# Performance work log

Hardware: AMD Instinct MI355X
Metric: run time of the kernel (lower is better)

The kernel has to match this reference:

```python
import jax, jax.numpy as jnp
import numpy as np

WCNT, EMB, H, T, B = 50000, 25, 25, 200, 4096


def setup_inputs() -> dict:
    key = jax.random.key(0)
    ks = jax.random.split(key, 12)
    s = 1.0 / np.sqrt(H)  # PyTorch GRU init range

    def u(k, shape):
        return jax.random.uniform(k, shape, minval=-s, maxval=s, dtype=jnp.float32)

    emb = jax.random.normal(ks[1], (WCNT, EMB), dtype=jnp.float32)
    emb = emb.at[0].set(0.0)  # padding_idx=0
    return {
        "input": jax.random.randint(ks[0], (T, B), 0, WCNT),
        "hidden": jnp.zeros((2, B, H), jnp.float32),
        "emb": emb,
        "w_ih_f": u(ks[2], (3 * H, EMB)), "w_hh_f": u(ks[3], (3 * H, H)),
        "b_ih_f": u(ks[4], (3 * H,)),     "b_hh_f": u(ks[5], (3 * H,)),
        "w_ih_b": u(ks[6], (3 * H, EMB)), "w_hh_b": u(ks[7], (3 * H, H)),
        "b_ih_b": u(ks[8], (3 * H,)),     "b_hh_b": u(ks[9], (3 * H,)),
    }


def _gru_dir(x, h0, w_ih, w_hh, b_ih, b_hh, reverse):
    # Precompute input-gate projections for all timesteps: [T, B, 3H]
    xg = jnp.einsum('tbi,gi->tbg', x, w_ih) + b_ih

    def step(h, xg_t):
        gh = h @ w_hh.T + b_hh
        xr, xz, xn = jnp.split(xg_t, 3, axis=-1)
        hr, hz, hn = jnp.split(gh, 3, axis=-1)
        r = jax.nn.sigmoid(xr + hr)
        z = jax.nn.sigmoid(xz + hz)
        n = jnp.tanh(xn + r * hn)
        h_new = (1.0 - z) * n + z * h
        return h_new, h_new

    hT, ys = jax.lax.scan(step, h0, xg, reverse=reverse)
    return ys, hT  # ys in original time order even when reversed


def reference(input, hidden, emb,
              w_ih_f, w_hh_f, b_ih_f, b_hh_f,
              w_ih_b, w_hh_b, b_ih_b, b_hh_b):
    emb_eff = emb.at[0].set(0.0)          # padding_idx=0
    x = emb_eff[input]                    # [T, B, EMB]
    yf, hf = _gru_dir(x, hidden[0], w_ih_f, w_hh_f, b_ih_f, b_hh_f, False)
    yb, hb = _gru_dir(x, hidden[1], w_ih_b, w_hh_b, b_ih_b, b_hh_b, True)
    y = jnp.concatenate([yf, yb], axis=-1)  # [T, B, 2H]
    y = jnp.max(y, axis=0)                  # max over time -> [B, 2H]
    h = jnp.stack([hf, hb], axis=0)         # [2, B, H]
    return (y, h)
```

## Files before the change

kernel.cpp:

```cpp
#include <hip/hip_runtime.h>
#include <cstddef>

#define T_LEN 200
#define BATCH 4096
#define EMBD  25
#define HD    25
#define WCNT  50000

__device__ __forceinline__ float frcp(float x) {
#if __has_builtin(__builtin_amdgcn_rcpf)
    return __builtin_amdgcn_rcpf(x);
#else
    return 1.0f / x;
#endif
}

__device__ __forceinline__ float fsig(float x) {
    float e = __expf(-x);
    return frcp(1.0f + e);
}
__device__ __forceinline__ float ftanh_(float x) {
    float e = __expf(-2.0f * x);
    return (1.0f - e) * frcp(1.0f + e);
}

__global__ __launch_bounds__(256) void embp_kernel(
    const float* __restrict__ emb,
    const float* __restrict__ w_ih_f, const float* __restrict__ b_ih_f,
    const float* __restrict__ w_ih_b, const float* __restrict__ b_ih_b,
    float* __restrict__ embP)
{
    int tid = blockIdx.x * 256 + threadIdx.x;
    if (tid >= 2 * WCNT * HD) return;
    int i   = tid % HD;
    int w   = (tid / HD) % WCNT;
    int dir = tid / (HD * WCNT);
    const float* wih = dir ? w_ih_b : w_ih_f;
    const float* bih = dir ? b_ih_b : b_ih_f;
    const float* er  = emb + (size_t)w * EMBD;
    const float* w0  = wih + (0 * HD + i) * EMBD;
    const float* w1  = wih + (1 * HD + i) * EMBD;
    const float* w2  = wih + (2 * HD + i) * EMBD;
    float a0 = bih[i], a1 = bih[HD + i], a2 = bih[2 * HD + i];
    #pragma unroll
    for (int j = 0; j < EMBD; ++j) {
        float x = er[j];
        a0 = fmaf(w0[j], x, a0);
        a1 = fmaf(w1[j], x, a1);
        a2 = fmaf(w2[j], x, a2);
    }
    float* o = embP + ((size_t)dir * WCNT + w) * 75;
    o[i] = a0; o[i + 25] = a1; o[i + 50] = a2;
}

template<bool USE_EMBP>
__global__ __launch_bounds__(256) void gru_kernel(
    const int*   __restrict__ input,
    const float* __restrict__ hidden,
    const float* __restrict__ emb,
    const float* __restrict__ w_hh_f, const float* __restrict__ b_hh_f,
    const float* __restrict__ w_ih_f, const float* __restrict__ b_ih_f,
    const float* __restrict__ w_hh_b, const float* __restrict__ b_hh_b,
    const float* __restrict__ w_ih_b, const float* __restrict__ b_ih_b,
    const float* __restrict__ embP,
    float* __restrict__ out)
{
    __shared__ float4 hsh4[8][7];
    __shared__ float4 xsh4[8][7];
    float* hshf = (float*)hsh4;
    float* xshf = (float*)xsh4;

    const int wave = threadIdx.x >> 6;
    const int half = (threadIdx.x >> 5) & 1;
    const int sub  = threadIdx.x & 31;
    const int b    = blockIdx.x * 4 + wave;
    const int dir  = half;
    const int csub = sub < 25 ? sub : 0;
    const int c    = wave * 2 + half;

    const float* whh = dir ? w_hh_b : w_hh_f;
    const float* bhh = dir ? b_hh_b : b_hh_f;
    const float* wih = dir ? w_ih_b : w_ih_f;
    const float* bih = dir ? b_ih_b : b_ih_f;

    float wg0[28], wg1[28], wg2[28];
    #pragma unroll
    for (int j = 0; j < 28; ++j) {
        wg0[j] = (j < 25) ? whh[(0 * 25 + csub) * 25 + j] : 0.0f;
        wg1[j] = (j < 25) ? whh[(1 * 25 + csub) * 25 + j] : 0.0f;
        wg2[j] = (j < 25) ? whh[(2 * 25 + csub) * 25 + j] : 0.0f;
    }
    const float bh0 = bhh[csub], bh1 = bhh[25 + csub], bh2 = bhh[50 + csub];

    float wi0[28], wi1[28], wi2[28];
    float bx0 = 0.f, bx1 = 0.f, bx2 = 0.f;
    if constexpr (!USE_EMBP) {
        #pragma unroll
        for (int j = 0; j < 28; ++j) {
            wi0[j] = (j < 25) ? wih[(0 * 25 + csub) * 25 + j] : 0.0f;
            wi1[j] = (j < 25) ? wih[(1 * 25 + csub) * 25 + j] : 0.0f;
            wi2[j] = (j < 25) ? wih[(2 * 25 + csub) * 25 + j] : 0.0f;
        }
        bx0 = bih[csub]; bx1 = bih[25 + csub]; bx2 = bih[50 + csub];
    }

    float h0 = 0.0f;
    if (sub < 25) h0 = hidden[((size_t)dir * BATCH + b) * HD + sub];
    if (sub < 28) hshf[c * 28 + sub] = (sub < 25) ? h0 : 0.0f;
    if constexpr (!USE_EMBP) {
        if (sub >= 25 && sub < 28) xshf[c * 28 + sub] = 0.0f;
    }
    __syncthreads();

    const int* ipt = input + (dir ? (T_LEN - 1) * BATCH : 0) + b;
    const int  istr = dir ? -BATCH : BATCH;

    int idx_c = ipt[0];
    int idx_n = ipt[istr];

    const size_t dirW = (size_t)dir * WCNT;
    float xgc0 = 0.f, xgc1 = 0.f, xgc2 = 0.f, xcur = 0.f;
    if constexpr (USE_EMBP) {
        const float* gp = embP + (dirW + (size_t)idx_c) * 75;
        xgc0 = gp[csub]; xgc1 = gp[csub + 25]; xgc2 = gp[csub + 50];
    } else {
        xcur = emb[(size_t)idx_c * EMBD + csub];
    }

    float hown = h0;
    float ymax = -3.0e38f;

    #pragma unroll 2
    for (int tt = 0; tt < T_LEN; ++tt) {
        int t2 = (tt + 2 < T_LEN) ? tt + 2 : T_LEN - 1;
        int idx_n2 = ipt[t2 * istr];

        float xgn0 = 0.f, xgn1 = 0.f, xgn2 = 0.f, xnext = 0.f;
        if constexpr (USE_EMBP) {
            const float* gp = embP + (dirW + (size_t)idx_n) * 75;
            xgn0 = gp[csub]; xgn1 = gp[csub + 25]; xgn2 = gp[csub + 50];
        } else {
            xnext = emb[(size_t)idx_n * EMBD + csub];
            __builtin_amdgcn_wave_barrier();
            if (sub < 25) xshf[c * 28 + sub] = xcur;
            __builtin_amdgcn_wave_barrier();
        }

        float ar = bh0, az = bh1, an = bh2;
        float axr = bx0, axz = bx1, axn = bx2;
        #pragma unroll
        for (int jb = 0; jb < 7; ++jb) {
            float4 hv = hsh4[c][jb];
            ar = fmaf(wg0[4*jb+0], hv.x, ar); ar = fmaf(wg0[4*jb+1], hv.y, ar);
            ar = fmaf(wg0[4*jb+2], hv.z, ar); ar = fmaf(wg0[4*jb+3], hv.w, ar);
            az = fmaf(wg1[4*jb+0], hv.x, az); az = fmaf(wg1[4*jb+1], hv.y, az);
            az = fmaf(wg1[4*jb+2], hv.z, az); az = fmaf(wg1[4*jb+3], hv.w, az);
            an = fmaf(wg2[4*jb+0], hv.x, an); an = fmaf(wg2[4*jb+1], hv.y, an);
            an = fmaf(wg2[4*jb+2], hv.z, an); an = fmaf(wg2[4*jb+3], hv.w, an);
            if constexpr (!USE_EMBP) {
                float4 xv = xsh4[c][jb];
                axr = fmaf(wi0[4*jb+0], xv.x, axr); axr = fmaf(wi0[4*jb+1], xv.y, axr);
                axr = fmaf(wi0[4*jb+2], xv.z, axr); axr = fmaf(wi0[4*jb+3], xv.w, axr);
                axz = fmaf(wi1[4*jb+0], xv.x, axz); axz = fmaf(wi1[4*jb+1], xv.y, axz);
                axz = fmaf(wi1[4*jb+2], xv.z, axz); axz = fmaf(wi1[4*jb+3], xv.w, axz);
                axn = fmaf(wi2[4*jb+0], xv.x, axn); axn = fmaf(wi2[4*jb+1], xv.y, axn);
                axn = fmaf(wi2[4*jb+2], xv.z, axn); axn = fmaf(wi2[4*jb+3], xv.w, axn);
            }
        }

        float pr, pz, pn_pre;
        if constexpr (USE_EMBP) { pr = xgc0 + ar; pz = xgc1 + az; }
        else                    { pr = axr + ar;  pz = axz + az; }
        float r = fsig(pr);
        float z = fsig(pz);
        if constexpr (USE_EMBP) pn_pre = fmaf(r, an, xgc2);
        else                    pn_pre = fmaf(r, an, axn);
        float n = ftanh_(pn_pre);
        float hnew = fmaf(z, hown - n, n);
        ymax = fmaxf(ymax, hnew);

        __builtin_amdgcn_wave_barrier();
        if (sub < 25) hshf[c * 28 + sub] = hnew;
        __builtin_amdgcn_wave_barrier();

        hown = hnew;
        xgc0 = xgn0; xgc1 = xgn1; xgc2 = xgn2; xcur = xnext;
        idx_c = idx_n; idx_n = idx_n2;
    }

    if (sub < 25) {
        out[(size_t)b * 50 + dir * 25 + sub] = ymax;
        out[204800 + ((size_t)dir * BATCH + b) * HD + sub] = hown;
    }
}

extern "C" void kernel_launch(void* const* d_in, const int* in_sizes, int n_in,
                              void* d_out, int out_size, void* d_ws, size_t ws_size,
                              hipStream_t stream) {
    const int*   input  = (const int*)  d_in[0];
    const float* hidden = (const float*)d_in[1];
    const float* emb    = (const float*)d_in[2];
    const float* w_ih_f = (const float*)d_in[3];
    const float* w_hh_f = (const float*)d_in[4];
    const float* b_ih_f = (const float*)d_in[5];
    const float* b_hh_f = (const float*)d_in[6];
    const float* w_ih_b = (const float*)d_in[7];
    const float* w_hh_b = (const float*)d_in[8];
    const float* b_ih_b = (const float*)d_in[9];
    const float* b_hh_b = (const float*)d_in[10];
    float* out = (float*)d_out;

    const size_t embp_bytes = (size_t)2 * WCNT * 75 * sizeof(float);
    if (ws_size >= embp_bytes) {
        float* embP = (float*)d_ws;
        int total = 2 * WCNT * HD;
        embp_kernel<<<(total + 255) / 256, 256, 0, stream>>>(
            emb, w_ih_f, b_ih_f, w_ih_b, b_ih_b, embP);
        gru_kernel<true><<<BATCH / 4, 256, 0, stream>>>(
            input, hidden, emb,
            w_hh_f, b_hh_f, w_ih_f, b_ih_f,
            w_hh_b, b_hh_b, w_ih_b, b_ih_b,
            embP, out);
    } else {
        gru_kernel<false><<<BATCH / 4, 256, 0, stream>>>(
            input, hidden, emb,
            w_hh_f, b_hh_f, w_ih_f, b_ih_f,
            w_hh_b, b_hh_b, w_ih_b, b_ih_b,
            nullptr, out);
    }
}
```

Baseline: 280.2 us.

## Interleave gate projections in embP and deepen gather prefetch in GRU kernel

The precomputed input-projection table is re-laid out so the three gate values for each hidden unit sit next to each other, letting each lane read 12 contiguous bytes instead of three strided loads. The recurrent kernel is split into a dedicated embP version that prefetches table rows two steps ahead and index values four steps ahead to hide gather latency. It drops the zero-padded 28-wide weight arrays to 25 entries and adds occupancy launch bounds. This uses more registers for the deeper pipeline, and the tail element is handled by a separate scalar LDS read.

```diff
diff --git a/kernel.cpp b/kernel.cpp
--- a/kernel.cpp
+++ b/kernel.cpp
@@ -49,12 +49,116 @@
         a1 = fmaf(w1[j], x, a1);
         a2 = fmaf(w2[j], x, a2);
     }
-    float* o = embP + ((size_t)dir * WCNT + w) * 75;
-    o[i] = a0; o[i + 25] = a1; o[i + 50] = a2;
-}
-
-template<bool USE_EMBP>
-__global__ __launch_bounds__(256) void gru_kernel(
+    float* o = embP + ((size_t)dir * WCNT + w) * 75 + i * 3;
+    o[0] = a0; o[1] = a1; o[2] = a2;
+}
+
+__global__ __launch_bounds__(256, 4) void gru_embp_kernel(
+    const int*   __restrict__ input,
+    const float* __restrict__ hidden,
+    const float* __restrict__ w_hh_f, const float* __restrict__ b_hh_f,
+    const float* __restrict__ w_hh_b, const float* __restrict__ b_hh_b,
+    const float* __restrict__ embP,
+    float* __restrict__ out)
+{
+    __shared__ float hsh[8][28];
+
+    const int wave = threadIdx.x >> 6;
+    const int half = (threadIdx.x >> 5) & 1;
+    const int sub  = threadIdx.x & 31;
+    const int b    = blockIdx.x * 4 + wave;
+    const int dir  = half;
+    const int csub = sub < 25 ? sub : 0;
+    const int c    = wave * 2 + half;
+
+    const float* whh = dir ? w_hh_b : w_hh_f;
+    const float* bhh = dir ? b_hh_b : b_hh_f;
+
+    float wg0[25], wg1[25], wg2[25];
+    #pragma unroll
+    for (int j = 0; j < 25; ++j) {
+        wg0[j] = whh[(0 * 25 + csub) * 25 + j];
+        wg1[j] = whh[(1 * 25 + csub) * 25 + j];
+        wg2[j] = whh[(2 * 25 + csub) * 25 + j];
+    }
+    const float bh0 = bhh[csub], bh1 = bhh[25 + csub], bh2 = bhh[50 + csub];
+
+    float h0 = 0.0f;
+    if (sub < 25) h0 = hidden[((size_t)dir * BATCH + b) * HD + sub];
+    if (sub < 25) hsh[c][sub] = h0;
+    __syncthreads();
+
+    const int* ipt  = input + (dir ? (T_LEN - 1) * BATCH : 0) + b;
+    const int  istr = dir ? -BATCH : BATCH;
+
+    int ia = ipt[0];
+    int ib_ = ipt[istr];
+    int ic = ipt[2 * istr];
+    int id_ = ipt[3 * istr];
+
+    const float* tbl = embP + (size_t)dir * WCNT * 75 + csub * 3;
+
+    float xa0, xa1, xa2, xb0, xb1, xb2;
+    {
+        const float* p = tbl + (size_t)ia * 75;
+        xa0 = p[0]; xa1 = p[1]; xa2 = p[2];
+        const float* q = tbl + (size_t)ib_ * 75;
+        xb0 = q[0]; xb1 = q[1]; xb2 = q[2];
+    }
+
+    float hown = h0;
+    float ymax = -3.0e38f;
+    const float4* h4 = (const float4*)(&hsh[c][0]);
+
+    #pragma unroll 2
+    for (int tt = 0; tt < T_LEN; ++tt) {
+        float xc0, xc1, xc2;
+        {
+            const float* p = tbl + (size_t)ic * 75;
+            xc0 = p[0]; xc1 = p[1]; xc2 = p[2];
+        }
+        ic = id_;
+        int t4 = (tt + 4 < T_LEN) ? tt + 4 : T_LEN - 1;
+        id_ = ipt[t4 * istr];
+
+        float ar = bh0, az = bh1, an = bh2;
+        #pragma unroll
+        for (int jb = 0; jb < 6; ++jb) {
+            float4 hv = h4[jb];
+            ar = fmaf(wg0[4*jb+0], hv.x, ar); ar = fmaf(wg0[4*jb+1], hv.y, ar);
+            ar = fmaf(wg0[4*jb+2], hv.z, ar); ar = fmaf(wg0[4*jb+3], hv.w, ar);
+            az = fmaf(wg1[4*jb+0], hv.x, az); az = fmaf(wg1[4*jb+1], hv.y, az);
+            az = fmaf(wg1[4*jb+2], hv.z, az); az = fmaf(wg1[4*jb+3], hv.w, az);
+            an = fmaf(wg2[4*jb+0], hv.x, an); an = fmaf(wg2[4*jb+1], hv.y, an);
+            an = fmaf(wg2[4*jb+2], hv.z, an); an = fmaf(wg2[4*jb+3], hv.w, an);
+        }
+        float h24 = hsh[c][24];
+        ar = fmaf(wg0[24], h24, ar);
+        az = fmaf(wg1[24], h24, az);
+        an = fmaf(wg2[24], h24, an);
+
+        float r = fsig(xa0 + ar);
+        float z = fsig(xa1 + az);
+        float n = ftanh_(fmaf(r, an, xa2));
+        float hnew = fmaf(z, hown - n, n);
+        ymax = fmaxf(ymax, hnew);
+
+        __builtin_amdgcn_wave_barrier();
+        if (sub < 25) hsh[c][sub] = hnew;
+        __builtin_amdgcn_wave_barrier();
+
+        hown = hnew;
+        xa0 = xb0; xa1 = xb1; xa2 = xb2;
+        xb0 = xc0; xb1 = xc1; xb2 = xc2;
+    }
+
+    if (sub < 25) {
+        out[(size_t)b * 50 + dir * 25 + sub] = ymax;
+        out[204800 + ((size_t)dir * BATCH + b) * HD + sub] = hown;
+    }
+}
+
+__global__ __launch_bounds__(256) void gru_fallback_kernel(
     const int*   __restrict__ input,
     const float* __restrict__ hidden,
     const float* __restrict__ emb,
@@ -62,7 +166,6 @@
     const float* __restrict__ w_ih_f, const float* __restrict__ b_ih_f,
     const float* __restrict__ w_hh_b, const float* __restrict__ b_hh_b,
     const float* __restrict__ w_ih_b, const float* __restrict__ b_ih_b,
-    const float* __restrict__ embP,
     float* __restrict__ out)
 {
     __shared__ float4 hsh4[8][7];
@@ -83,99 +186,66 @@
     const float* wih = dir ? w_ih_b : w_ih_f;
     const float* bih = dir ? b_ih_b : b_ih_f;
 
-    float wg0[28], wg1[28], wg2[28];
+    float wg0[28], wg1[28], wg2[28], wi0[28], wi1[28], wi2[28];
     #pragma unroll
     for (int j = 0; j < 28; ++j) {
         wg0[j] = (j < 25) ? whh[(0 * 25 + csub) * 25 + j] : 0.0f;
         wg1[j] = (j < 25) ? whh[(1 * 25 + csub) * 25 + j] : 0.0f;
         wg2[j] = (j < 25) ? whh[(2 * 25 + csub) * 25 + j] : 0.0f;
+        wi0[j] = (j < 25) ? wih[(0 * 25 + csub) * 25 + j] : 0.0f;
+        wi1[j] = (j < 25) ? wih[(1 * 25 + csub) * 25 + j] : 0.0f;
+        wi2[j] = (j < 25) ? wih[(2 * 25 + csub) * 25 + j] : 0.0f;
     }
     const float bh0 = bhh[csub], bh1 = bhh[25 + csub], bh2 = bhh[50 + csub];
-
-    float wi0[28], wi1[28], wi2[28];
-    float bx0 = 0.f, bx1 = 0.f, bx2 = 0.f;
-    if constexpr (!USE_EMBP) {
-        #pragma unroll
-        for (int j = 0; j < 28; ++j) {
-            wi0[j] = (j < 25) ? wih[(0 * 25 + csub) * 25 + j] : 0.0f;
-            wi1[j] = (j < 25) ? wih[(1 * 25 + csub) * 25 + j] : 0.0f;
-            wi2[j] = (j < 25) ? wih[(2 * 25 + csub) * 25 + j] : 0.0f;
-        }
-        bx0 = bih[csub]; bx1 = bih[25 + csub]; bx2 = bih[50 + csub];
-    }
+    const float bx0 = bih[csub], bx1 = bih[25 + csub], bx2 = bih[50 + csub];
 
     float h0 = 0.0f;
     if (sub < 25) h0 = hidden[((size_t)dir * BATCH + b) * HD + sub];
     if (sub < 28) hshf[c * 28 + sub] = (sub < 25) ? h0 : 0.0f;
-    if constexpr (!USE_EMBP) {
-        if (sub >= 25 && sub < 28) xshf[c * 28 + sub] = 0.0f;
-    }
+    if (sub >= 25 && sub < 28) xshf[c * 28 + sub] = 0.0f;
     __syncthreads();
 
-    const int* ipt = input + (dir ? (T_LEN - 1) * BATCH : 0) + b;
+    const int* ipt  = input + (dir ? (T_LEN - 1) * BATCH : 0) + b;
     const int  istr = dir ? -BATCH : BATCH;
 
     int idx_c = ipt[0];
     int idx_n = ipt[istr];
-
-    const size_t dirW = (size_t)dir * WCNT;
-    float xgc0 = 0.f, xgc1 = 0.f, xgc2 = 0.f, xcur = 0.f;
-    if constexpr (USE_EMBP) {
-        const float* gp = embP + (dirW + (size_t)idx_c) * 75;
-        xgc0 = gp[csub]; xgc1 = gp[csub + 25]; xgc2 = gp[csub + 50];
-    } else {
-        xcur = emb[(size_t)idx_c * EMBD + csub];
-    }
+    float xcur = emb[(size_t)idx_c * EMBD + csub];
 
     float hown = h0;
     float ymax = -3.0e38f;
 
-    #pragma unroll 2
     for (int tt = 0; tt < T_LEN; ++tt) {
         int t2 = (tt + 2 < T_LEN) ? tt + 2 : T_LEN - 1;
         int idx_n2 = ipt[t2 * istr];
-
-        float xgn0 = 0.f, xgn1 = 0.f, xgn2 = 0.f, xnext = 0.f;
-        if constexpr (USE_EMBP) {
-            const float* gp = embP + (dirW + (size_t)idx_n) * 75;
-            xgn0 = gp[csub]; xgn1 = gp[csub + 25]; xgn2 = gp[csub + 50];
-        } else {
-            xnext = emb[(size_t)idx_n * EMBD + csub];
-            __builtin_amdgcn_wave_barrier();
-            if (sub < 25) xshf[c * 28 + sub] = xcur;
-            __builtin_amdgcn_wave_barrier();
-        }
+        float xnext = emb[(size_t)idx_n * EMBD + csub];
+        __builtin_amdgcn_wave_barrier();
+        if (sub < 25) xshf[c * 28 + sub] = xcur;
+        __builtin_amdgcn_wave_barrier();
 
         float ar = bh0, az = bh1, an = bh2;
         float axr = bx0, axz = bx1, axn = bx2;
         #pragma unroll
         for (int jb = 0; jb < 7; ++jb) {
             float4 hv = hsh4[c][jb];
+            float4 xv = xsh4[c][jb];
             ar = fmaf(wg0[4*jb+0], hv.x, ar); ar = fmaf(wg0[4*jb+1], hv.y, ar);
             ar = fmaf(wg0[4*jb+2], hv.z, ar); ar = fmaf(wg0[4*jb+3], hv.w, ar);
             az = fmaf(wg1[4*jb+0], hv.x, az); az = fmaf(wg1[4*jb+1], hv.y, az);
             az = fmaf(wg1[4*jb+2], hv.z, az); az = fmaf(wg1[4*jb+3], hv.w, az);
             an = fmaf(wg2[4*jb+0], hv.x, an); an = fmaf(wg2[4*jb+1], hv.y, an);
             an = fmaf(wg2[4*jb+2], hv.z, an); an = fmaf(wg2[4*jb+3], hv.w, an);
-            if constexpr (!USE_EMBP) {
-                float4 xv = xsh4[c][jb];
-                axr = fmaf(wi0[4*jb+0], xv.x, axr); axr = fmaf(wi0[4*jb+1], xv.y, axr);
-                axr = fmaf(wi0[4*jb+2], xv.z, axr); axr = fmaf(wi0[4*jb+3], xv.w, axr);
-                axz = fmaf(wi1[4*jb+0], xv.x, axz); axz = fmaf(wi1[4*jb+1], xv.y, axz);
-                axz = fmaf(wi1[4*jb+2], xv.z, axz); axz = fmaf(wi1[4*jb+3], xv.w, axz);
-                axn = fmaf(wi2[4*jb+0], xv.x, axn); axn = fmaf(wi2[4*jb+1], xv.y, axn);
-                axn = fmaf(wi2[4*jb+2], xv.z, axn); axn = fmaf(wi2[4*jb+3], xv.w, axn);
-            }
+            axr = fmaf(wi0[4*jb+0], xv.x, axr); axr = fmaf(wi0[4*jb+1], xv.y, axr);
+            axr = fmaf(wi0[4*jb+2], xv.z, axr); axr = fmaf(wi0[4*jb+3], xv.w, axr);
+            axz = fmaf(wi1[4*jb+0], xv.x, axz); axz = fmaf(wi1[4*jb+1], xv.y, axz);
+            axz = fmaf(wi1[4*jb+2], xv.z, axz); axz = fmaf(wi1[4*jb+3], xv.w, axz);
+            axn = fmaf(wi2[4*jb+0], xv.x, axn); axn = fmaf(wi2[4*jb+1], xv.y, axn);
+            axn = fmaf(wi2[4*jb+2], xv.z, axn); axn = fmaf(wi2[4*jb+3], xv.w, axn);
         }
 
-        float pr, pz, pn_pre;
-        if constexpr (USE_EMBP) { pr = xgc0 + ar; pz = xgc1 + az; }
-        else                    { pr = axr + ar;  pz = axz + az; }
-        float r = fsig(pr);
-        float z = fsig(pz);
-        if constexpr (USE_EMBP) pn_pre = fmaf(r, an, xgc2);
-        else                    pn_pre = fmaf(r, an, axn);
-        float n = ftanh_(pn_pre);
+        float r = fsig(axr + ar);
+        float z = fsig(axz + az);
+        float n = ftanh_(fmaf(r, an, axn));
         float hnew = fmaf(z, hown - n, n);
         ymax = fmaxf(ymax, hnew);
 
@@ -184,7 +254,7 @@
         __builtin_amdgcn_wave_barrier();
 
         hown = hnew;
-        xgc0 = xgn0; xgc1 = xgn1; xgc2 = xgn2; xcur = xnext;
+        xcur = xnext;
         idx_c = idx_n; idx_n = idx_n2;
     }
 
@@ -216,16 +286,15 @@
         int total = 2 * WCNT * HD;
         embp_kernel<<<(total + 255) / 256, 256, 0, stream>>>(
             emb, w_ih_f, b_ih_f, w_ih_b, b_ih_b, embP);
-        gru_kernel<true><<<BATCH / 4, 256, 0, stream>>>(
+        gru_embp_kernel<<<BATCH / 4, 256, 0, stream>>>(
+            input, hidden,
+            w_hh_f, b_hh_f, w_hh_b, b_hh_b,
+            embP, out);
+    } else {
+        gru_fallback_kernel<<<BATCH / 4, 256, 0, stream>>>(
             input, hidden, emb,
             w_hh_f, b_hh_f, w_ih_f, b_ih_f,
             w_hh_b, b_hh_b, w_ih_b, b_ih_b,
-            embP, out);
-    } else {
-        gru_kernel<false><<<BATCH / 4, 256, 0, stream>>>(
-            input, hidden, emb,
-            w_hh_f, b_hh_f, w_ih_f, b_ih_f,
-            w_hh_b, b_hh_b, w_ih_b, b_ih_b,
-            nullptr, out);
-    }
-}
+            out);
+    }
+}
```

After: 268.0 us. -4.4%, faster.
